# Kernel tuning notes

Measured on AMD Instinct MI355X. Metric: run time of the kernel, lower is better.

The kernel has to match this reference:

```python
import jax, jax.numpy as jnp
import numpy as np

E, B, C = 4, 262144, 128  # edge types, tokens, feature dim

def setup_inputs() -> dict:
    key = jax.random.key(0)
    k1, k2, k3 = jax.random.split(key, 3)
    xs = jax.random.normal(k1, (E, B, C), dtype=jnp.float32)
    Ws = jax.random.normal(k2, (E, C, C), dtype=jnp.float32) * (1.0 / np.sqrt(C))
    bs = jax.random.normal(k3, (E, C), dtype=jnp.float32) * 0.01
    return {"xs": xs, "Ws": Ws, "bs": bs}

def reference(xs, Ws, bs):
    # Per-edge-type op: y_e = xs[e] @ Ws[e] + bs[e]  (Linear per from_node type)
    # Aggregation: sum over edges.
    # Fused grouped form: contract over edge axis e and input channel c in one einsum.
    out = jnp.einsum('ebc,ecd->bd', xs, Ws)          # [B, C]
    out = out + bs.sum(axis=0)                       # bias from each edge op, summed by aggregation
    return out
```

## Files before the change

kernel.cpp:

```cpp
#include <hip/hip_runtime.h>

#define N_E 4
#define N_B 262144
#define N_C 128

typedef __attribute__((ext_vector_type(8))) short bf16x8;
typedef __attribute__((ext_vector_type(4))) float f32x4;
typedef __attribute__((ext_vector_type(4))) unsigned int u32x4;

__device__ __forceinline__ unsigned short f2bf(float f) {
  unsigned u = __float_as_uint(f);
  return (unsigned short)((u + 0x7FFFu + ((u >> 16) & 1u)) >> 16);
}

__global__ void __launch_bounds__(512)
grouped_gemm(const float* __restrict__ xs, const float* __restrict__ Ws,
             const float* __restrict__ bs, float* __restrict__ out) {
  __shared__ unsigned short lds_w[16 * 128 * 8];
  __shared__ float lds_bias[128];

  const int tid  = threadIdx.x;
  const int lane = tid & 63;
  const int wave = tid >> 6;
  const int l15  = lane & 15;
  const int hi   = lane >> 4;

  const int waveRow = blockIdx.x * 128 + wave * 16;

  if (tid < 128) {
    lds_bias[tid] = bs[tid] + bs[128 + tid] + bs[256 + tid] + bs[384 + tid];
  }

  f32x4 acc[8];
#pragma unroll
  for (int n = 0; n < 8; ++n) {
    f32x4 z = {0.0f, 0.0f, 0.0f, 0.0f};
    acc[n] = z;
  }

  const float* xrow_base = xs + (size_t)(waveRow + l15) * N_C;

  for (int e = 0; e < N_E; ++e) {
    __syncthreads();

    {
      const float* We = Ws + (size_t)e * N_C * N_C;
#pragma unroll
      for (int i = 0; i < 4; ++i) {
        int n = tid + i * 512;
        int u = n >> 7;
        int d = n & 127;
        const float* src = We + u * 8 * N_C + d;
        float v[8];
#pragma unroll
        for (int j = 0; j < 8; ++j) v[j] = src[j * N_C];
        u32x4 pk;
#pragma unroll
        for (int j = 0; j < 4; ++j)
          pk[j] = (unsigned)f2bf(v[2 * j]) | ((unsigned)f2bf(v[2 * j + 1]) << 16);
        *reinterpret_cast<u32x4*>(&lds_w[n * 8]) = pk;
      }
    }
    __syncthreads();

    const float* xrow = xrow_base + (size_t)e * N_B * N_C;
#pragma unroll
    for (int kt = 0; kt < 4; ++kt) {
      const float* ap = xrow + kt * 32 + hi * 8;
      f32x4 a0 = *reinterpret_cast<const f32x4*>(ap);
      f32x4 a1 = *reinterpret_cast<const f32x4*>(ap + 4);
      bf16x8 afrag;
#pragma unroll
      for (int j = 0; j < 4; ++j) {
        afrag[j]     = (short)f2bf(a0[j]);
        afrag[4 + j] = (short)f2bf(a1[j]);
      }
      const unsigned short* wbase = &lds_w[(size_t)((kt * 4 + hi) * 128 + l15) * 8];
#pragma unroll
      for (int n = 0; n < 8; ++n) {
        bf16x8 bfrag = *reinterpret_cast<const bf16x8*>(wbase + (size_t)n * 16 * 8);
        acc[n] = __builtin_amdgcn_mfma_f32_16x16x32_bf16(afrag, bfrag, acc[n], 0, 0, 0);
      }
    }
  }

#pragma unroll
  for (int n = 0; n < 8; ++n) {
    int d = n * 16 + l15;
    float bias = lds_bias[d];
#pragma unroll
    for (int r = 0; r < 4; ++r) {
      int row = waveRow + hi * 4 + r;
      out[(size_t)row * N_C + d] = acc[n][r] + bias;
    }
  }
}

extern "C" void kernel_launch(void* const* d_in, const int* in_sizes, int n_in,
                              void* d_out, int out_size, void* d_ws, size_t ws_size,
                              hipStream_t stream) {
  const float* xs = (const float*)d_in[0];
  const float* Ws = (const float*)d_in[1];
  const float* bs = (const float*)d_in[2];
  float* out = (float*)d_out;

  dim3 grid(N_B / 128);
  dim3 block(512);
  hipLaunchKernelGGL(grouped_gemm, grid, block, 0, stream, xs, Ws, bs, out);
}
```

Measured before the change: 163.6 us.

## Stage all edge weights in LDS once and drop per-edge barriers

Each block now converts all four weight matrices to bf16 and stores them in a 128KB dynamic LDS buffer up front, with one barrier. This replaces the per-edge reload bracketed by two barriers, so each wave can stream its x rows across all edges without synchronisation. The change also switches to the packed hardware bf16 conversion intrinsic and unrolls the edge loop. The large LDS footprint limits occupancy to about one block per CU, even though launch bounds ask for two.

```diff
diff --git a/kernel.cpp b/kernel.cpp
--- a/kernel.cpp
+++ b/kernel.cpp
@@ -1,4 +1,5 @@
 #include <hip/hip_runtime.h>
+#include <hip/hip_bf16.h>
 
 #define N_E 4
 #define N_B 262144
@@ -8,16 +9,20 @@
 typedef __attribute__((ext_vector_type(4))) float f32x4;
 typedef __attribute__((ext_vector_type(4))) unsigned int u32x4;
 
-__device__ __forceinline__ unsigned short f2bf(float f) {
-  unsigned u = __float_as_uint(f);
-  return (unsigned short)((u + 0x7FFFu + ((u >> 16) & 1u)) >> 16);
+__device__ __forceinline__ unsigned pk2(float lo, float hi) {
+  float2 t; t.x = lo; t.y = hi;
+  __hip_bfloat162 h = __float22bfloat162_rn(t);
+  union { __hip_bfloat162 h; unsigned u; } c;
+  c.h = h;
+  return c.u;
 }
 
-__global__ void __launch_bounds__(512)
+__global__ void __launch_bounds__(512, 2)
 grouped_gemm(const float* __restrict__ xs, const float* __restrict__ Ws,
              const float* __restrict__ bs, float* __restrict__ out) {
-  __shared__ unsigned short lds_w[16 * 128 * 8];
-  __shared__ float lds_bias[128];
+  extern __shared__ unsigned char smem[];
+  unsigned short* lds_w  = (unsigned short*)smem;
+  float*          lds_bias = (float*)(smem + N_E * 16 * 128 * 16);
 
   const int tid  = threadIdx.x;
   const int lane = tid & 63;
@@ -25,11 +30,27 @@
   const int l15  = lane & 15;
   const int hi   = lane >> 4;
 
-  const int waveRow = blockIdx.x * 128 + wave * 16;
-
+#pragma unroll
+  for (int i = 0; i < 16; ++i) {
+    int m = tid + i * 512;
+    int e = m >> 11;
+    int u = (m >> 7) & 15;
+    int d = m & 127;
+    const float* src = Ws + e * (N_C * N_C) + u * 8 * N_C + d;
+    float v[8];
+#pragma unroll
+    for (int j = 0; j < 8; ++j) v[j] = src[j * N_C];
+    u32x4 pk;
+#pragma unroll
+    for (int j = 0; j < 4; ++j) pk[j] = pk2(v[2 * j], v[2 * j + 1]);
+    *reinterpret_cast<u32x4*>(&lds_w[(size_t)m * 8]) = pk;
+  }
   if (tid < 128) {
     lds_bias[tid] = bs[tid] + bs[128 + tid] + bs[256 + tid] + bs[384 + tid];
   }
+  __syncthreads();
+
+  const int waveRow = blockIdx.x * 128 + wave * 16;
 
   f32x4 acc[8];
 #pragma unroll
@@ -38,47 +59,26 @@
     acc[n] = z;
   }
 
-  const float* xrow_base = xs + (size_t)(waveRow + l15) * N_C;
+  const float* xrow = xs + (size_t)(waveRow + l15) * N_C;
 
+#pragma unroll
   for (int e = 0; e < N_E; ++e) {
-    __syncthreads();
-
-    {
-      const float* We = Ws + (size_t)e * N_C * N_C;
-#pragma unroll
-      for (int i = 0; i < 4; ++i) {
-        int n = tid + i * 512;
-        int u = n >> 7;
-        int d = n & 127;
-        const float* src = We + u * 8 * N_C + d;
-        float v[8];
-#pragma unroll
-        for (int j = 0; j < 8; ++j) v[j] = src[j * N_C];
-        u32x4 pk;
-#pragma unroll
-        for (int j = 0; j < 4; ++j)
-          pk[j] = (unsigned)f2bf(v[2 * j]) | ((unsigned)f2bf(v[2 * j + 1]) << 16);
-        *reinterpret_cast<u32x4*>(&lds_w[n * 8]) = pk;
-      }
-    }
-    __syncthreads();
-
-    const float* xrow = xrow_base + (size_t)e * N_B * N_C;
+    const float* xe = xrow + (size_t)e * N_B * N_C;
 #pragma unroll
     for (int kt = 0; kt < 4; ++kt) {
-      const float* ap = xrow + kt * 32 + hi * 8;
+      const float* ap = xe + kt * 32 + hi * 8;
       f32x4 a0 = *reinterpret_cast<const f32x4*>(ap);
       f32x4 a1 = *reinterpret_cast<const f32x4*>(ap + 4);
       bf16x8 afrag;
-#pragma unroll
-      for (int j = 0; j < 4; ++j) {
-        afrag[j]     = (short)f2bf(a0[j]);
-        afrag[4 + j] = (short)f2bf(a1[j]);
-      }
-      const unsigned short* wbase = &lds_w[(size_t)((kt * 4 + hi) * 128 + l15) * 8];
+      unsigned* au = reinterpret_cast<unsigned*>(&afrag);
+      au[0] = pk2(a0[0], a0[1]);
+      au[1] = pk2(a0[2], a0[3]);
+      au[2] = pk2(a1[0], a1[1]);
+      au[3] = pk2(a1[2], a1[3]);
+      const unsigned short* wb = &lds_w[(size_t)((e * 16 + kt * 4 + hi) * 128 + l15) * 8];
 #pragma unroll
       for (int n = 0; n < 8; ++n) {
-        bf16x8 bfrag = *reinterpret_cast<const bf16x8*>(wbase + (size_t)n * 16 * 8);
+        bf16x8 bfrag = *reinterpret_cast<const bf16x8*>(wb + (size_t)n * 16 * 8);
         acc[n] = __builtin_amdgcn_mfma_f32_16x16x32_bf16(afrag, bfrag, acc[n], 0, 0, 0);
       }
     }
@@ -104,7 +104,11 @@
   const float* bs = (const float*)d_in[2];
   float* out = (float*)d_out;
 
+  const size_t smem = (size_t)N_E * 16 * 128 * 16 + 128 * sizeof(float);
+  hipFuncSetAttribute((const void*)grouped_gemm,
+                      hipFuncAttributeMaxDynamicSharedMemorySize, (int)smem);
+
   dim3 grid(N_B / 128);
   dim3 block(512);
-  hipLaunchKernelGGL(grouped_gemm, grid, block, 0, stream, xs, Ws, bs, out);
+  hipLaunchKernelGGL(grouped_gemm, grid, block, smem, stream, xs, Ws, bs, out);
 }
```

Result: no change. 163.8 us (+0.1%).
